# Kernel tuning notes

Hardware: AMD Instinct MI355X
Metric: run time of the kernel (lower is better)

Reference implementation:

```python
import jax, jax.numpy as jnp
import numpy as np

EPS = 1e-8

def _penalty(v, lo, hi):
    # if v<lo: (lo-v)/lo ; elif v>hi (hi finite): (v-hi)/hi ; else 0
    below = (lo - v) / lo
    if np.isinf(hi):
        return jnp.where(v < lo, below, 0.0)
    above = (v - hi) / hi
    return jnp.where(v < lo, below, jnp.where(v > hi, above, 0.0))

def _symbolic_features(x):
    # x: [B, input_dim]; column mapping from the original per-row loop
    am, bod, do, ph, nit = x[:, 0], x[:, 1], x[:, 2], x[:, 4], x[:, 7]
    # penalties in param_order = [ph, ammonia, bod, dissolved_oxygen, nitrate]
    p_ph  = _penalty(ph, 6.5, 8.5)
    p_am  = _penalty(am, 0.001, 0.5)
    p_bod = _penalty(bod, 0.001, 5.0)
    p_do  = _penalty(do, 6.0, np.inf)
    p_nit = _penalty(nit, 0.001, 10.0)
    # pollutant scores (missing params like 'nitrogen'/'orthophosphate' are skipped -> count adjusts)
    s_bact = (1.2 * am / (0.5 + EPS) + 1.5 * bod / (5.0 + EPS) - 0.8 * do / (10.0 + EPS)) / 3.0
    s_chem = (1.5 * ph / (8.5 + EPS) + 1.0 * nit / (10.0 + EPS)) / 2.0
    s_org  = (2.0 * bod / (5.0 + EPS) - 1.5 * do / (10.0 + EPS) + 0.8 * am / (0.5 + EPS)) / 3.0
    s_agr  = (2.0 * nit / (10.0 + EPS)) / 1.0
    resil = 1.0 / (1.0 + (p_ph + p_am + p_bod + p_do + p_nit) + EPS)
    return jnp.stack([p_ph, p_am, p_bod, p_do, p_nit, s_bact, s_chem, s_org, s_agr, resil], axis=1)

def setup_inputs() -> dict:
    key = jax.random.key(0)
    ks = jax.random.split(key, 16)
    B, D_IN, SYM, H = 1048576, 10, 10, 64
    def lin(k, fin, fout):
        k1, k2 = jax.random.split(k)
        s = 1.0 / np.sqrt(fin)
        return (jax.random.uniform(k1, (fin, fout), jnp.float32, -s, s),
                jax.random.uniform(k2, (fout,), jnp.float32, -s, s))
    W_sym, b_sym = lin(ks[0], SYM, H // 2)
    W_in, b_in = lin(ks[1], D_IN + H // 2, H)
    W1, b1 = lin(ks[2], H, H)
    W2, b2 = lin(ks[3], H, H)
    W3, b3 = lin(ks[4], H, H)
    W_r1, b_r1 = lin(ks[5], H, H // 2)
    W_r2, b_r2 = lin(ks[6], H // 2, 1)
    W_c1, b_c1 = lin(ks[7], H, H // 2)
    W_c2, b_c2 = lin(ks[8], H // 2, 4)
    x = jax.random.uniform(ks[9], (B, D_IN), jnp.float32)
    return {"x": x, "W_sym": W_sym, "b_sym": b_sym, "W_in": W_in, "b_in": b_in,
            "W1": W1, "b1": b1, "W2": W2, "b2": b2, "W3": W3, "b3": b3,
            "W_r1": W_r1, "b_r1": b_r1, "W_r2": W_r2, "b_r2": b_r2,
            "W_c1": W_c1, "b_c1": b_c1, "W_c2": W_c2, "b_c2": b_c2}

def reference(x, W_sym, b_sym, W_in, b_in, W1, b1, W2, b2, W3, b3,
              W_r1, b_r1, W_r2, b_r2, W_c1, b_c1, W_c2, b_c2):
    elu = jax.nn.elu
    sym = _symbolic_features(x)                      # [B, 10]
    sym_enc = elu(sym @ W_sym + b_sym)               # [B, 32]  (Dropout: eval mode = identity)
    h = elu(jnp.concatenate([x, sym_enc], axis=1) @ W_in + b_in)  # [B, 64]
    for W, b in ((W1, b1), (W2, b2), (W3, b3)):
        h = h + elu(h @ W + b)                       # residual MLP stack
    predictions = elu(h @ W_r1 + b_r1) @ W_r2 + b_r2            # [B, 1]
    pollutant_logits = elu(h @ W_c1 + b_c1) @ W_c2 + b_c2       # [B, 4]
    return predictions, pollutant_logits
```

## Files before the change

### kernel.cpp

```cpp
#include <hip/hip_runtime.h>
#include <hip/hip_bf16.h>
#include <math.h>

#define NROWS 1048576
#define EPSF 1e-8f

typedef unsigned short ushortT;
typedef __attribute__((ext_vector_type(8))) short short8;
typedef __attribute__((ext_vector_type(4))) short short4v;
typedef __attribute__((ext_vector_type(4))) float floatx4;
typedef __attribute__((ext_vector_type(2))) int int2v;

#define WS_HI   256
#define WS_LO   41216
#define WS_MF   82176
#define MF_B5   0
#define MF_WSYM 320
#define MF_BSYM 640
#define MF_WR2  672
#define MF_BR2  704
#define MF_WC2  708
#define MF_BC2  836
#define MF_WC2T 840

#define LDS_FENCE() asm volatile("s_waitcnt lgkmcnt(0)" ::: "memory")

struct WPtrs { const void* p[19]; };

__global__ void sniff_kernel(const ushortT* __restrict__ x, int* __restrict__ flag) {
    if (threadIdx.x == 0 && blockIdx.x == 0) {
        unsigned s = 0;
        for (int i = 0; i < 64; ++i) s |= (unsigned)(x[i] & 0x8000u);
        *flag = s ? 1 : 0;
    }
}

__device__ __forceinline__ float ldw(const void* p, int i, bool f32) {
    return f32 ? ((const float*)p)[i]
               : __uint_as_float(((unsigned)((const ushortT*)p)[i]) << 16);
}

__global__ void prep_kernel(WPtrs wp, const int* __restrict__ flag, void* __restrict__ ws) {
    const bool f32 = (*flag != 0);
    ushortT* hi = (ushortT*)((char*)ws + WS_HI);
    ushortT* lo = (ushortT*)((char*)ws + WS_LO);
    float* mf = (float*)((char*)ws + WS_MF);
    const int B = blockIdx.x;
    if (B < 5) {
        const int L = B;
        for (int idx = threadIdx.x; idx < 4096; idx += 256) {
            const int j8 = idx & 7, ln = (idx >> 3) & 63, s2 = (idx >> 9) & 1, t = idx >> 10;
            const int s = 2 * s2 + (j8 >> 2), j = j8 & 3;
            const int k = 16 * s + 4 * (ln >> 4) + j;
            const int m = 16 * t + (ln & 15);
            float w = 0.0f;
            if (L == 0)      { if (k < 42) w = ldw(wp.p[3], k * 64 + m, f32); }
            else if (L <= 3) { if (k < 64) w = ldw(wp.p[3 + 2 * L], k * 64 + m, f32); }
            else             { if (k < 64) w = (m < 32) ? ldw(wp.p[11], k * 32 + m, f32)
                                                        : ldw(wp.p[15], k * 32 + (m - 32), f32); }
            const unsigned u = __float_as_uint(w);
            const float rem = w - __uint_as_float(u & 0xffff0000u);
            hi[L * 4096 + idx] = (ushortT)(u >> 16);
            lo[L * 4096 + idx] = (ushortT)(__float_as_uint(rem) >> 16);
        }
    } else {
        const int src[12] = {4, 6, 8, 10, 12, 16, 1, 2, 13, 14, 17, 18};
        const int cnt[12] = {64, 64, 64, 64, 32, 32, 320, 32, 32, 1, 128, 4};
        const int dst[12] = {0, 64, 128, 192, 256, 288, MF_WSYM, MF_BSYM, MF_WR2, MF_BR2, MF_WC2, MF_BC2};
        for (int a = 0; a < 12; ++a)
            for (int i = threadIdx.x; i < cnt[a]; i += 256)
                mf[dst[a] + i] = ldw(wp.p[src[a]], i, f32);
        for (int i = threadIdx.x; i < 128; i += 256) {
            const int qq = i >> 5, j = i & 31;
            mf[MF_WC2T + i] = ldw(wp.p[17], j * 4 + qq, f32);
        }
    }
}

__device__ __forceinline__ float eluf(float v) {
    return fmaxf(v, 0.0f) + (__expf(fminf(v, 0.0f)) - 1.0f);
}

__device__ __forceinline__ unsigned pack_hi16(unsigned ua, unsigned ub) {
    return __builtin_amdgcn_perm(ub, ua, 0x07060302u);
}

__device__ __forceinline__ float b2f(short h) {
    return __uint_as_float(((unsigned)(ushortT)h) << 16);
}

__device__ __forceinline__ void split4(float a0, float a1, float a2, float a3,
                                       short4v& h4, short4v& l4) {
    const unsigned u0 = __float_as_uint(a0), u1 = __float_as_uint(a1);
    const unsigned u2 = __float_as_uint(a2), u3 = __float_as_uint(a3);
    int2v h, l;
    h[0] = (int)pack_hi16(u0, u1);
    h[1] = (int)pack_hi16(u2, u3);
    const float l0 = a0 - __uint_as_float(u0 & 0xffff0000u);
    const float l1 = a1 - __uint_as_float(u1 & 0xffff0000u);
    const float l2 = a2 - __uint_as_float(u2 & 0xffff0000u);
    const float l3 = a3 - __uint_as_float(u3 & 0xffff0000u);
    l[0] = (int)pack_hi16(__float_as_uint(l0), __float_as_uint(l1));
    l[1] = (int)pack_hi16(__float_as_uint(l2), __float_as_uint(l3));
    h4 = __builtin_bit_cast(short4v, h);
    l4 = __builtin_bit_cast(short4v, l);
}

__device__ __forceinline__ floatx4 mfma16(short4v a, short4v b, floatx4 c) {
#if __has_builtin(__builtin_amdgcn_mfma_f32_16x16x16bf16_1k)
    return __builtin_amdgcn_mfma_f32_16x16x16bf16_1k(a, b, c, 0, 0, 0);
#else
    floatx4 d;
    asm("v_mfma_f32_16x16x16_bf16 %0, %1, %2, %3" : "=v"(d) : "v"(a), "v"(b), "v"(c));
    return d;
#endif
}

template<bool F32>
__device__ __forceinline__ void run_body(
    const void* __restrict__ xin, const char* __restrict__ wsb,
    void* __restrict__ out, float (* __restrict__ hb)[68],
    const int lane, const int rowbase)
{
    const ushortT* __restrict__ wfhi = (const ushortT*)(wsb + WS_HI);
    const ushortT* __restrict__ wflo = (const ushortT*)(wsb + WS_LO);
    const float* __restrict__ mf = (const float*)(wsb + WS_MF);
    const int n = lane & 15, q = lane >> 4;

    short4v Bhi[2][4], Blo[2][4];

    #pragma unroll
    for (int u = 0; u < 2; ++u) {
        const int rowg = rowbase + 16 * u + n;
        float x[10];
        if (F32) {
            const float* xp = (const float*)xin + (size_t)rowg * 10;
            #pragma unroll
            for (int i = 0; i < 10; ++i) x[i] = xp[i];
        } else {
            const unsigned* xd = (const unsigned*)((const ushortT*)xin + (size_t)rowg * 10);
            #pragma unroll
            for (int i = 0; i < 5; ++i) {
                const unsigned d = xd[i];
                x[2 * i]     = __uint_as_float(d << 16);
                x[2 * i + 1] = __uint_as_float(d & 0xffff0000u);
            }
        }
        if (q == 0) {
            #pragma unroll
            for (int i = 0; i < 10; ++i) hb[n][i] = x[i];
        }
        if (u == 0) {
            #pragma unroll
            for (int i = 0; i < 6; ++i) {
                const int c = 42 + q * 6 + i;
                if (c < 64) hb[n][c] = 0.0f;
            }
        }

        const float am = x[0], bod = x[1], dox = x[2], ph = x[4], nit = x[7];
        const float p_ph  = ph  < 6.5f   ? (6.5f - ph) * 0.15384616f
                          : (ph > 8.5f   ? (ph - 8.5f) * 0.11764706f : 0.0f);
        const float p_am  = am  < 0.001f ? (0.001f - am) * 1000.0f
                          : (am > 0.5f   ? (am - 0.5f) * 2.0f : 0.0f);
        const float p_bod = bod < 0.001f ? (0.001f - bod) * 1000.0f
                          : (bod > 5.0f  ? (bod - 5.0f) * 0.2f : 0.0f);
        const float p_do  = dox < 6.0f   ? (6.0f - dox) * 0.16666667f : 0.0f;
        const float p_nit = nit < 0.001f ? (0.001f - nit) * 1000.0f
                          : (nit > 10.0f ? (nit - 10.0f) * 0.1f : 0.0f);
        const float s_bact = (am * 2.3999999f + bod * 0.29999998f - dox * 0.08f) * 0.33333334f;
        const float s_chem = (ph * 0.17647059f + nit * 0.1f) * 0.5f;
        const float s_org  = (bod * 0.39999998f - dox * 0.14999999f + am * 1.5999999f) * 0.33333334f;
        const float s_agr  = nit * 0.2f;
        const float resil  = 1.0f / (1.0f + (p_ph + p_am + p_bod + p_do + p_nit) + EPSF);
        const float sym[10] = {p_ph, p_am, p_bod, p_do, p_nit, s_bact, s_chem, s_org, s_agr, resil};

        float se[8];
        {
            const floatx4 b0 = *(const floatx4*)(mf + MF_BSYM + q * 8);
            const floatx4 b1 = *(const floatx4*)(mf + MF_BSYM + q * 8 + 4);
            #pragma unroll
            for (int jj = 0; jj < 4; ++jj) { se[jj] = b0[jj]; se[4 + jj] = b1[jj]; }
            #pragma unroll
            for (int k = 0; k < 10; ++k) {
                const floatx4 w0 = *(const floatx4*)(mf + MF_WSYM + k * 32 + q * 8);
                const floatx4 w1 = *(const floatx4*)(mf + MF_WSYM + k * 32 + q * 8 + 4);
                #pragma unroll
                for (int jj = 0; jj < 4; ++jj) {
                    se[jj]     = fmaf(sym[k], w0[jj], se[jj]);
                    se[4 + jj] = fmaf(sym[k], w1[jj], se[4 + jj]);
                }
            }
        }
        #pragma unroll
        for (int jj = 0; jj < 8; ++jj) hb[n][10 + q * 8 + jj] = eluf(se[jj]);
        LDS_FENCE();

        #pragma unroll
        for (int s = 0; s < 4; ++s) {
            const floatx4 v = *(const floatx4*)&hb[n][16 * s + 4 * q];
            split4(v[0], v[1], v[2], v[3], Bhi[u][s], Blo[u][s]);
        }
        LDS_FENCE();
    }

    #pragma unroll
    for (int L = 0; L < 5; ++L) {
        short8 Ap[8];
        const int base = L * 4096 + lane * 8;
        #pragma unroll
        for (int c = 0; c < 8; ++c)
            Ap[c] = *(const short8*)(wfhi + base + c * 512);
        short8 Alp[8];
        if (F32) {
            #pragma unroll
            for (int c = 0; c < 8; ++c)
                Alp[c] = *(const short8*)(wflo + base + c * 512);
        }

        floatx4 acc[2][4];
        #pragma unroll
        for (int t = 0; t < 4; ++t) {
            const floatx4 b = *(const floatx4*)(mf + MF_B5 + L * 64 + 16 * t + 4 * q);
            acc[0][t] = b; acc[1][t] = b;
        }
        #pragma unroll
        for (int t = 0; t < 4; ++t) {
            #pragma unroll
            for (int s2 = 0; s2 < 2; ++s2) {
                const short8 A = Ap[t * 2 + s2];
                const short4v ae = {A[0], A[1], A[2], A[3]};
                const short4v ao = {A[4], A[5], A[6], A[7]};
                #pragma unroll
                for (int u = 0; u < 2; ++u) {
                    acc[u][t] = mfma16(ae, Bhi[u][2 * s2],     acc[u][t]);
                    acc[u][t] = mfma16(ae, Blo[u][2 * s2],     acc[u][t]);
                    acc[u][t] = mfma16(ao, Bhi[u][2 * s2 + 1], acc[u][t]);
                    acc[u][t] = mfma16(ao, Blo[u][2 * s2 + 1], acc[u][t]);
                }
                if (F32) {
                    const short8 Al = Alp[t * 2 + s2];
                    const short4v le  = {Al[0], Al[1], Al[2], Al[3]};
                    const short4v lo_ = {Al[4], Al[5], Al[6], Al[7]};
                    #pragma unroll
                    for (int u = 0; u < 2; ++u) {
                        acc[u][t] = mfma16(le,  Bhi[u][2 * s2],     acc[u][t]);
                        acc[u][t] = mfma16(lo_, Bhi[u][2 * s2 + 1], acc[u][t]);
                    }
                }
            }
        }

        if (L < 4) {
            #pragma unroll
            for (int u = 0; u < 2; ++u) {
                #pragma unroll
                for (int t = 0; t < 4; ++t) {
                    float h[4];
                    #pragma unroll
                    for (int r = 0; r < 4; ++r) {
                        float e = eluf(acc[u][t][r]);
                        if (L >= 1) e += b2f(Bhi[u][t][r]) + b2f(Blo[u][t][r]);
                        h[r] = e;
                    }
                    split4(h[0], h[1], h[2], h[3], Bhi[u][t], Blo[u][t]);
                }
            }
        } else {
            const floatx4 wr0 = *(const floatx4*)(mf + MF_WR2 + 4 * q);
            const floatx4 wr1 = *(const floatx4*)(mf + MF_WR2 + 16 + 4 * q);
            floatx4 wc0[4], wc1[4];
            #pragma unroll
            for (int c = 0; c < 4; ++c) {
                wc0[c] = *(const floatx4*)(mf + MF_WC2T + c * 32 + 4 * q);
                wc1[c] = *(const floatx4*)(mf + MF_WC2T + c * 32 + 16 + 4 * q);
            }
            #pragma unroll
            for (int u = 0; u < 2; ++u) {
                float pred = (q == 0) ? mf[MF_BR2] : 0.0f;
                float z2[4], z3[4];
                #pragma unroll
                for (int r = 0; r < 4; ++r) {
                    pred = fmaf(eluf(acc[u][0][r]), wr0[r], pred);
                    pred = fmaf(eluf(acc[u][1][r]), wr1[r], pred);
                    z2[r] = eluf(acc[u][2][r]);
                    z3[r] = eluf(acc[u][3][r]);
                }
                float lg[4];
                #pragma unroll
                for (int c = 0; c < 4; ++c) {
                    float l = (q == 0) ? mf[MF_BC2 + c] : 0.0f;
                    #pragma unroll
                    for (int r = 0; r < 4; ++r) {
                        l = fmaf(z2[r], wc0[c][r], l);
                        l = fmaf(z3[r], wc1[c][r], l);
                    }
                    lg[c] = l;
                }
                pred += __shfl_xor(pred, 16, 64);
                pred += __shfl_xor(pred, 32, 64);
                #pragma unroll
                for (int c = 0; c < 4; ++c) {
                    lg[c] += __shfl_xor(lg[c], 16, 64);
                    lg[c] += __shfl_xor(lg[c], 32, 64);
                }
                const float lsel = q == 0 ? lg[0] : (q == 1 ? lg[1] : (q == 2 ? lg[2] : lg[3]));
                const int rowg = rowbase + 16 * u + n;
                if (F32) {
                    float* o = (float*)out;
                    if (q == 0) o[rowg] = pred;
                    o[NROWS + rowg * 4 + q] = lsel;
                } else {
                    __hip_bfloat16* o = (__hip_bfloat16*)out;
                    if (q == 0) o[rowg] = __float2bfloat16(pred);
                    o[NROWS + rowg * 4 + q] = __float2bfloat16(lsel);
                }
            }
        }
    }
}

__global__ __launch_bounds__(256, 2) void mlp_mfma_kernel(
    const void* __restrict__ xin, const int* __restrict__ flagp,
    const void* __restrict__ ws, void* __restrict__ out)
{
    __shared__ float hball[4][16][68];
    const int tid = threadIdx.x;
    const int wave = tid >> 6, lane = tid & 63;
    const int rowbase = blockIdx.x * 128 + wave * 32;
    if (*flagp != 0)
        run_body<true>(xin, (const char*)ws, out, hball[wave], lane, rowbase);
    else
        run_body<false>(xin, (const char*)ws, out, hball[wave], lane, rowbase);
}

extern "C" void kernel_launch(void* const* d_in, const int* in_sizes, int n_in,
                              void* d_out, int out_size, void* d_ws, size_t ws_size,
                              hipStream_t stream) {
    (void)in_sizes; (void)n_in; (void)out_size; (void)ws_size;
    int* flag = (int*)d_ws;

    sniff_kernel<<<1, 64, 0, stream>>>((const ushortT*)d_in[0], flag);

    WPtrs wp;
    for (int i = 0; i < 19; ++i) wp.p[i] = d_in[i];
    prep_kernel<<<6, 256, 0, stream>>>(wp, flag, d_ws);

    mlp_mfma_kernel<<<NROWS / 128, 256, 0, stream>>>(d_in[0], flag, d_ws, d_out);
}
```

Before: 371.6 us.

## Make MLP kernel persistent with LDS-resident weights and prefetched inputs

Switches from one 32-row tile per wave over 8192 blocks to a persistent grid of 512 blocks, where each wave processes 16 tiles. Each block stages the bf16 hi weights and the small fp32 parameters into LDS once and reuses them across iterations, instead of reloading them from global memory for every tile. The next tile's input rows are prefetched while the current tile computes. The residual is now kept as an fp32 value rather than rebuilt from the split bf16 pair. The LDS footprint grows to about 62 KB per block, which may limit occupancy, and the fixed grid gives less parallelism if the row count changes.

```diff
diff --git a/kernel.cpp b/kernel.cpp
--- a/kernel.cpp
+++ b/kernel.cpp
@@ -4,6 +4,9 @@
 
 #define NROWS 1048576
 #define EPSF 1e-8f
+#define GRID 512
+#define TPB 256
+#define ITERS 16
 
 typedef unsigned short ushortT;
 typedef __attribute__((ext_vector_type(8))) short short8;
@@ -22,6 +25,7 @@
 #define MF_WC2  708
 #define MF_BC2  836
 #define MF_WC2T 840
+#define MF_TOTAL 968
 
 #define LDS_FENCE() asm volatile("s_waitcnt lgkmcnt(0)" ::: "memory")
 
@@ -85,10 +89,6 @@
     return __builtin_amdgcn_perm(ub, ua, 0x07060302u);
 }
 
-__device__ __forceinline__ float b2f(short h) {
-    return __uint_as_float(((unsigned)(ushortT)h) << 16);
-}
-
 __device__ __forceinline__ void split4(float a0, float a1, float a2, float a3,
                                        short4v& h4, short4v& l4) {
     const unsigned u0 = __float_as_uint(a0), u1 = __float_as_uint(a1);
@@ -119,219 +119,263 @@
 template<bool F32>
 __device__ __forceinline__ void run_body(
     const void* __restrict__ xin, const char* __restrict__ wsb,
-    void* __restrict__ out, float (* __restrict__ hb)[68],
-    const int lane, const int rowbase)
+    void* __restrict__ out,
+    const ushortT* __restrict__ wlds,
+    const float* __restrict__ mflds,
+    float (* __restrict__ hb)[68],
+    const int lane, const int wavebase)
 {
-    const ushortT* __restrict__ wfhi = (const ushortT*)(wsb + WS_HI);
     const ushortT* __restrict__ wflo = (const ushortT*)(wsb + WS_LO);
-    const float* __restrict__ mf = (const float*)(wsb + WS_MF);
     const int n = lane & 15, q = lane >> 4;
 
-    short4v Bhi[2][4], Blo[2][4];
-
+    #pragma unroll
+    for (int i = 0; i < 6; ++i) {
+        const int c = 42 + q * 6 + i;
+        if (c < 64) hb[n][c] = 0.0f;
+    }
+
+    unsigned xu[2][5];
+    float xf[2][10];
     #pragma unroll
     for (int u = 0; u < 2; ++u) {
-        const int rowg = rowbase + 16 * u + n;
-        float x[10];
+        const int rowg = wavebase + 16 * u + n;
         if (F32) {
             const float* xp = (const float*)xin + (size_t)rowg * 10;
             #pragma unroll
-            for (int i = 0; i < 10; ++i) x[i] = xp[i];
+            for (int i = 0; i < 10; ++i) xf[u][i] = xp[i];
         } else {
             const unsigned* xd = (const unsigned*)((const ushortT*)xin + (size_t)rowg * 10);
             #pragma unroll
-            for (int i = 0; i < 5; ++i) {
-                const unsigned d = xd[i];
-                x[2 * i]     = __uint_as_float(d << 16);
-                x[2 * i + 1] = __uint_as_float(d & 0xffff0000u);
-            }
-        }
-        if (q == 0) {
-            #pragma unroll
-            for (int i = 0; i < 10; ++i) hb[n][i] = x[i];
-        }
-        if (u == 0) {
-            #pragma unroll
-            for (int i = 0; i < 6; ++i) {
-                const int c = 42 + q * 6 + i;
-                if (c < 64) hb[n][c] = 0.0f;
-            }
-        }
-
-        const float am = x[0], bod = x[1], dox = x[2], ph = x[4], nit = x[7];
-        const float p_ph  = ph  < 6.5f   ? (6.5f - ph) * 0.15384616f
-                          : (ph > 8.5f   ? (ph - 8.5f) * 0.11764706f : 0.0f);
-        const float p_am  = am  < 0.001f ? (0.001f - am) * 1000.0f
-                          : (am > 0.5f   ? (am - 0.5f) * 2.0f : 0.0f);
-        const float p_bod = bod < 0.001f ? (0.001f - bod) * 1000.0f
-                          : (bod > 5.0f  ? (bod - 5.0f) * 0.2f : 0.0f);
-        const float p_do  = dox < 6.0f   ? (6.0f - dox) * 0.16666667f : 0.0f;
-        const float p_nit = nit < 0.001f ? (0.001f - nit) * 1000.0f
-                          : (nit > 10.0f ? (nit - 10.0f) * 0.1f : 0.0f);
-        const float s_bact = (am * 2.3999999f + bod * 0.29999998f - dox * 0.08f) * 0.33333334f;
-        const float s_chem = (ph * 0.17647059f + nit * 0.1f) * 0.5f;
-        const float s_org  = (bod * 0.39999998f - dox * 0.14999999f + am * 1.5999999f) * 0.33333334f;
-        const float s_agr  = nit * 0.2f;
-        const float resil  = 1.0f / (1.0f + (p_ph + p_am + p_bod + p_do + p_nit) + EPSF);
-        const float sym[10] = {p_ph, p_am, p_bod, p_do, p_nit, s_bact, s_chem, s_org, s_agr, resil};
-
-        float se[8];
+            for (int i = 0; i < 5; ++i) xu[u][i] = xd[i];
+        }
+    }
+
+    #pragma unroll 1
+    for (int it = 0; it < ITERS; ++it) {
+        const int rowbase = wavebase + it * 32;
+        short4v Bhi[2][4], Blo[2][4];
+
+        #pragma unroll
+        for (int u = 0; u < 2; ++u) {
+            float x[10];
+            if (F32) {
+                #pragma unroll
+                for (int i = 0; i < 10; ++i) x[i] = xf[u][i];
+            } else {
+                #pragma unroll
+                for (int i = 0; i < 5; ++i) {
+                    const unsigned d = xu[u][i];
+                    x[2 * i]     = __uint_as_float(d << 16);
+                    x[2 * i + 1] = __uint_as_float(d & 0xffff0000u);
+                }
+            }
+            if (q == 0) {
+                #pragma unroll
+                for (int i = 0; i < 10; ++i) hb[n][i] = x[i];
+            }
+
+            const float am = x[0], bod = x[1], dox = x[2], ph = x[4], nit = x[7];
+            const float p_ph  = ph  < 6.5f   ? (6.5f - ph) * 0.15384616f
+                              : (ph > 8.5f   ? (ph - 8.5f) * 0.11764706f : 0.0f);
+            const float p_am  = am  < 0.001f ? (0.001f - am) * 1000.0f
+                              : (am > 0.5f   ? (am - 0.5f) * 2.0f : 0.0f);
+            const float p_bod = bod < 0.001f ? (0.001f - bod) * 1000.0f
+                              : (bod > 5.0f  ? (bod - 5.0f) * 0.2f : 0.0f);
+            const float p_do  = dox < 6.0f   ? (6.0f - dox) * 0.16666667f : 0.0f;
+            const float p_nit = nit < 0.001f ? (0.001f - nit) * 1000.0f
+                              : (nit > 10.0f ? (nit - 10.0f) * 0.1f : 0.0f);
+            const float s_bact = (am * 2.3999999f + bod * 0.29999998f - dox * 0.08f) * 0.33333334f;
+            const float s_chem = (ph * 0.17647059f + nit * 0.1f) * 0.5f;
+            const float s_org  = (bod * 0.39999998f - dox * 0.14999999f + am * 1.5999999f) * 0.33333334f;
+            const float s_agr  = nit * 0.2f;
+            const float resil  = 1.0f / (1.0f + (p_ph + p_am + p_bod + p_do + p_nit) + EPSF);
+            const float sym[10] = {p_ph, p_am, p_bod, p_do, p_nit, s_bact, s_chem, s_org, s_agr, resil};
+
+            float se[8];
+            {
+                const floatx4 b0 = *(const floatx4*)(mflds + MF_BSYM + q * 8);
+                const floatx4 b1 = *(const floatx4*)(mflds + MF_BSYM + q * 8 + 4);
+                #pragma unroll
+                for (int jj = 0; jj < 4; ++jj) { se[jj] = b0[jj]; se[4 + jj] = b1[jj]; }
+                #pragma unroll
+                for (int k = 0; k < 10; ++k) {
+                    const floatx4 w0 = *(const floatx4*)(mflds + MF_WSYM + k * 32 + q * 8);
+                    const floatx4 w1 = *(const floatx4*)(mflds + MF_WSYM + k * 32 + q * 8 + 4);
+                    #pragma unroll
+                    for (int jj = 0; jj < 4; ++jj) {
+                        se[jj]     = fmaf(sym[k], w0[jj], se[jj]);
+                        se[4 + jj] = fmaf(sym[k], w1[jj], se[4 + jj]);
+                    }
+                }
+            }
+            #pragma unroll
+            for (int jj = 0; jj < 8; ++jj) hb[n][10 + q * 8 + jj] = eluf(se[jj]);
+            LDS_FENCE();
+            #pragma unroll
+            for (int s = 0; s < 4; ++s) {
+                const floatx4 v = *(const floatx4*)&hb[n][16 * s + 4 * q];
+                split4(v[0], v[1], v[2], v[3], Bhi[u][s], Blo[u][s]);
+            }
+            LDS_FENCE();
+        }
+
         {
-            const floatx4 b0 = *(const floatx4*)(mf + MF_BSYM + q * 8);
-            const floatx4 b1 = *(const floatx4*)(mf + MF_BSYM + q * 8 + 4);
-            #pragma unroll
-            for (int jj = 0; jj < 4; ++jj) { se[jj] = b0[jj]; se[4 + jj] = b1[jj]; }
-            #pragma unroll
-            for (int k = 0; k < 10; ++k) {
-                const floatx4 w0 = *(const floatx4*)(mf + MF_WSYM + k * 32 + q * 8);
-                const floatx4 w1 = *(const floatx4*)(mf + MF_WSYM + k * 32 + q * 8 + 4);
-                #pragma unroll
-                for (int jj = 0; jj < 4; ++jj) {
-                    se[jj]     = fmaf(sym[k], w0[jj], se[jj]);
-                    se[4 + jj] = fmaf(sym[k], w1[jj], se[4 + jj]);
-                }
-            }
-        }
+            const int itn = (it + 1 < ITERS) ? it + 1 : it;
+            #pragma unroll
+            for (int u = 0; u < 2; ++u) {
+                const int rowg = wavebase + itn * 32 + 16 * u + n;
+                if (F32) {
+                    const float* xp = (const float*)xin + (size_t)rowg * 10;
+                    #pragma unroll
+                    for (int i = 0; i < 10; ++i) xf[u][i] = xp[i];
+                } else {
+                    const unsigned* xd = (const unsigned*)((const ushortT*)xin + (size_t)rowg * 10);
+                    #pragma unroll
+                    for (int i = 0; i < 5; ++i) xu[u][i] = xd[i];
+                }
+            }
+        }
+
+        float hprev[2][4][4];
         #pragma unroll
-        for (int jj = 0; jj < 8; ++jj) hb[n][10 + q * 8 + jj] = eluf(se[jj]);
-        LDS_FENCE();
-
-        #pragma unroll
-        for (int s = 0; s < 4; ++s) {
-            const floatx4 v = *(const floatx4*)&hb[n][16 * s + 4 * q];
-            split4(v[0], v[1], v[2], v[3], Bhi[u][s], Blo[u][s]);
-        }
-        LDS_FENCE();
-    }
-
-    #pragma unroll
-    for (int L = 0; L < 5; ++L) {
-        short8 Ap[8];
-        const int base = L * 4096 + lane * 8;
-        #pragma unroll
-        for (int c = 0; c < 8; ++c)
-            Ap[c] = *(const short8*)(wfhi + base + c * 512);
-        short8 Alp[8];
-        if (F32) {
+        for (int L = 0; L < 5; ++L) {
+            short8 Ap[8];
+            const ushortT* wl = wlds + L * 4096 + lane * 8;
             #pragma unroll
             for (int c = 0; c < 8; ++c)
-                Alp[c] = *(const short8*)(wflo + base + c * 512);
-        }
-
-        floatx4 acc[2][4];
-        #pragma unroll
-        for (int t = 0; t < 4; ++t) {
-            const floatx4 b = *(const floatx4*)(mf + MF_B5 + L * 64 + 16 * t + 4 * q);
-            acc[0][t] = b; acc[1][t] = b;
-        }
-        #pragma unroll
-        for (int t = 0; t < 4; ++t) {
-            #pragma unroll
-            for (int s2 = 0; s2 < 2; ++s2) {
-                const short8 A = Ap[t * 2 + s2];
-                const short4v ae = {A[0], A[1], A[2], A[3]};
-                const short4v ao = {A[4], A[5], A[6], A[7]};
+                Ap[c] = *(const short8*)(wl + c * 512);
+            short8 Alp[8];
+            if (F32) {
+                const int base = L * 4096 + lane * 8;
+                #pragma unroll
+                for (int c = 0; c < 8; ++c)
+                    Alp[c] = *(const short8*)(wflo + base + c * 512);
+            }
+
+            floatx4 acc[2][4];
+            #pragma unroll
+            for (int t = 0; t < 4; ++t) {
+                const floatx4 b = *(const floatx4*)(mflds + MF_B5 + L * 64 + 16 * t + 4 * q);
+                acc[0][t] = b; acc[1][t] = b;
+            }
+            #pragma unroll
+            for (int t = 0; t < 4; ++t) {
+                #pragma unroll
+                for (int s2 = 0; s2 < 2; ++s2) {
+                    const short8 A = Ap[t * 2 + s2];
+                    const short4v ae = {A[0], A[1], A[2], A[3]};
+                    const short4v ao = {A[4], A[5], A[6], A[7]};
+                    #pragma unroll
+                    for (int u = 0; u < 2; ++u) {
+                        acc[u][t] = mfma16(ae, Bhi[u][2 * s2],     acc[u][t]);
+                        acc[u][t] = mfma16(ae, Blo[u][2 * s2],     acc[u][t]);
+                        acc[u][t] = mfma16(ao, Bhi[u][2 * s2 + 1], acc[u][t]);
+                        acc[u][t] = mfma16(ao, Blo[u][2 * s2 + 1], acc[u][t]);
+                    }
+                    if (F32) {
+                        const short8 Al = Alp[t * 2 + s2];
+                        const short4v le  = {Al[0], Al[1], Al[2], Al[3]};
+                        const short4v lo_ = {Al[4], Al[5], Al[6], Al[7]};
+                        #pragma unroll
+                        for (int u = 0; u < 2; ++u) {
+                            acc[u][t] = mfma16(le,  Bhi[u][2 * s2],     acc[u][t]);
+                            acc[u][t] = mfma16(lo_, Bhi[u][2 * s2 + 1], acc[u][t]);
+                        }
+                    }
+                }
+            }
+
+            if (L < 4) {
                 #pragma unroll
                 for (int u = 0; u < 2; ++u) {
-                    acc[u][t] = mfma16(ae, Bhi[u][2 * s2],     acc[u][t]);
-                    acc[u][t] = mfma16(ae, Blo[u][2 * s2],     acc[u][t]);
-                    acc[u][t] = mfma16(ao, Bhi[u][2 * s2 + 1], acc[u][t]);
-                    acc[u][t] = mfma16(ao, Blo[u][2 * s2 + 1], acc[u][t]);
-                }
-                if (F32) {
-                    const short8 Al = Alp[t * 2 + s2];
-                    const short4v le  = {Al[0], Al[1], Al[2], Al[3]};
-                    const short4v lo_ = {Al[4], Al[5], Al[6], Al[7]};
-                    #pragma unroll
-                    for (int u = 0; u < 2; ++u) {
-                        acc[u][t] = mfma16(le,  Bhi[u][2 * s2],     acc[u][t]);
-                        acc[u][t] = mfma16(lo_, Bhi[u][2 * s2 + 1], acc[u][t]);
-                    }
-                }
-            }
-        }
-
-        if (L < 4) {
-            #pragma unroll
-            for (int u = 0; u < 2; ++u) {
-                #pragma unroll
-                for (int t = 0; t < 4; ++t) {
-                    float h[4];
+                    #pragma unroll
+                    for (int t = 0; t < 4; ++t) {
+                        #pragma unroll
+                        for (int r = 0; r < 4; ++r) {
+                            float e = eluf(acc[u][t][r]);
+                            if (L >= 1) e += hprev[u][t][r];
+                            hprev[u][t][r] = e;
+                        }
+                        split4(hprev[u][t][0], hprev[u][t][1],
+                               hprev[u][t][2], hprev[u][t][3], Bhi[u][t], Blo[u][t]);
+                    }
+                }
+            } else {
+                const floatx4 wr0 = *(const floatx4*)(mflds + MF_WR2 + 4 * q);
+                const floatx4 wr1 = *(const floatx4*)(mflds + MF_WR2 + 16 + 4 * q);
+                #pragma unroll
+                for (int u = 0; u < 2; ++u) {
+                    float pred = (q == 0) ? mflds[MF_BR2] : 0.0f;
+                    float z2[4], z3[4];
                     #pragma unroll
                     for (int r = 0; r < 4; ++r) {
-                        float e = eluf(acc[u][t][r]);
-                        if (L >= 1) e += b2f(Bhi[u][t][r]) + b2f(Blo[u][t][r]);
-                        h[r] = e;
-                    }
-                    split4(h[0], h[1], h[2], h[3], Bhi[u][t], Blo[u][t]);
-                }
-            }
-        } else {
-            const floatx4 wr0 = *(const floatx4*)(mf + MF_WR2 + 4 * q);
-            const floatx4 wr1 = *(const floatx4*)(mf + MF_WR2 + 16 + 4 * q);
-            floatx4 wc0[4], wc1[4];
-            #pragma unroll
-            for (int c = 0; c < 4; ++c) {
-                wc0[c] = *(const floatx4*)(mf + MF_WC2T + c * 32 + 4 * q);
-                wc1[c] = *(const floatx4*)(mf + MF_WC2T + c * 32 + 16 + 4 * q);
-            }
-            #pragma unroll
-            for (int u = 0; u < 2; ++u) {
-                float pred = (q == 0) ? mf[MF_BR2] : 0.0f;
-                float z2[4], z3[4];
-                #pragma unroll
-                for (int r = 0; r < 4; ++r) {
-                    pred = fmaf(eluf(acc[u][0][r]), wr0[r], pred);
-                    pred = fmaf(eluf(acc[u][1][r]), wr1[r], pred);
-                    z2[r] = eluf(acc[u][2][r]);
-                    z3[r] = eluf(acc[u][3][r]);
-                }
-                float lg[4];
-                #pragma unroll
-                for (int c = 0; c < 4; ++c) {
-                    float l = (q == 0) ? mf[MF_BC2 + c] : 0.0f;
-                    #pragma unroll
-                    for (int r = 0; r < 4; ++r) {
-                        l = fmaf(z2[r], wc0[c][r], l);
-                        l = fmaf(z3[r], wc1[c][r], l);
-                    }
-                    lg[c] = l;
-                }
-                pred += __shfl_xor(pred, 16, 64);
-                pred += __shfl_xor(pred, 32, 64);
-                #pragma unroll
-                for (int c = 0; c < 4; ++c) {
-                    lg[c] += __shfl_xor(lg[c], 16, 64);
-                    lg[c] += __shfl_xor(lg[c], 32, 64);
-                }
-                const float lsel = q == 0 ? lg[0] : (q == 1 ? lg[1] : (q == 2 ? lg[2] : lg[3]));
-                const int rowg = rowbase + 16 * u + n;
-                if (F32) {
-                    float* o = (float*)out;
-                    if (q == 0) o[rowg] = pred;
-                    o[NROWS + rowg * 4 + q] = lsel;
-                } else {
-                    __hip_bfloat16* o = (__hip_bfloat16*)out;
-                    if (q == 0) o[rowg] = __float2bfloat16(pred);
-                    o[NROWS + rowg * 4 + q] = __float2bfloat16(lsel);
-                }
-            }
-        }
-    }
-}
-
-__global__ __launch_bounds__(256, 2) void mlp_mfma_kernel(
+                        pred = fmaf(eluf(acc[u][0][r]), wr0[r], pred);
+                        pred = fmaf(eluf(acc[u][1][r]), wr1[r], pred);
+                        z2[r] = eluf(acc[u][2][r]);
+                        z3[r] = eluf(acc[u][3][r]);
+                    }
+                    float lg[4];
+                    #pragma unroll
+                    for (int c = 0; c < 4; ++c) {
+                        const floatx4 wc0 = *(const floatx4*)(mflds + MF_WC2T + c * 32 + 4 * q);
+                        const floatx4 wc1 = *(const floatx4*)(mflds + MF_WC2T + c * 32 + 16 + 4 * q);
+                        float l = (q == 0) ? mflds[MF_BC2 + c] : 0.0f;
+                        #pragma unroll
+                        for (int r = 0; r < 4; ++r) {
+                            l = fmaf(z2[r], wc0[r], l);
+                            l = fmaf(z3[r], wc1[r], l);
+                        }
+                        lg[c] = l;
+                    }
+                    pred += __shfl_xor(pred, 16, 64);
+                    pred += __shfl_xor(pred, 32, 64);
+                    #pragma unroll
+                    for (int c = 0; c < 4; ++c) {
+                        lg[c] += __shfl_xor(lg[c], 16, 64);
+                        lg[c] += __shfl_xor(lg[c], 32, 64);
+                    }
+                    const float lsel = q == 0 ? lg[0] : (q == 1 ? lg[1] : (q == 2 ? lg[2] : lg[3]));
+                    const int rowg = rowbase + 16 * u + n;
+                    if (F32) {
+                        float* o = (float*)out;
+                        if (q == 0) o[rowg] = pred;
+                        o[NROWS + rowg * 4 + q] = lsel;
+                    } else {
+                        __hip_bfloat16* o = (__hip_bfloat16*)out;
+                        if (q == 0) o[rowg] = __float2bfloat16(pred);
+                        o[NROWS + rowg * 4 + q] = __float2bfloat16(lsel);
+                    }
+                }
+            }
+        }
+    }
+}
+
+__global__ __launch_bounds__(TPB, 2) void mlp_mfma_kernel(
     const void* __restrict__ xin, const int* __restrict__ flagp,
     const void* __restrict__ ws, void* __restrict__ out)
 {
+    __shared__ __align__(16) ushortT wlds[5 * 4096];
+    __shared__ __align__(16) float mflds[MF_TOTAL];
     __shared__ float hball[4][16][68];
+
     const int tid = threadIdx.x;
+    {
+        const unsigned* src = (const unsigned*)((const char*)ws + WS_HI);
+        unsigned* dst = (unsigned*)wlds;
+        for (int i = tid; i < 10240; i += TPB) dst[i] = src[i];
+        const float* mfsrc = (const float*)((const char*)ws + WS_MF);
+        for (int i = tid; i < MF_TOTAL; i += TPB) mflds[i] = mfsrc[i];
+    }
+    __syncthreads();
+
     const int wave = tid >> 6, lane = tid & 63;
-    const int rowbase = blockIdx.x * 128 + wave * 32;
+    const int gw = blockIdx.x * 4 + wave;
+    const int wavebase = gw * (32 * ITERS);
     if (*flagp != 0)
-        run_body<true>(xin, (const char*)ws, out, hball[wave], lane, rowbase);
+        run_body<true>(xin, (const char*)ws, out, wlds, mflds, hball[wave], lane, wavebase);
     else
-        run_body<false>(xin, (const char*)ws, out, hball[wave], lane, rowbase);
+        run_body<false>(xin, (const char*)ws, out, wlds, mflds, hball[wave], lane, wavebase);
 }
 
 extern "C" void kernel_launch(void* const* d_in, const int* in_sizes, int n_in,
@@ -346,5 +390,5 @@
     for (int i = 0; i < 19; ++i) wp.p[i] = d_in[i];
     prep_kernel<<<6, 256, 0, stream>>>(wp, flag, d_ws);
 
-    mlp_mfma_kernel<<<NROWS / 128, 256, 0, stream>>>(d_in[0], flag, d_ws, d_out);
-}
+    mlp_mfma_kernel<<<GRID, TPB, 0, stream>>>(d_in[0], flag, d_ws, d_out);
+}
```

Measured after the change: 334.3 us. 10.0% less time.
